# Performance work log

Measured on AMD Instinct MI355X. Metric: run time of the kernel, lower is better.

The kernel has to match this reference:

```python
import jax, jax.numpy as jnp
import numpy as np

N, K = 256, 133
INPUT_W, INPUT_H = 256, 256
SPLIT = 2.0
W = round(INPUT_W * SPLIT)  # 512
H = round(INPUT_H * SPLIT)  # 512
SIGMA = (5.66, 5.66)
BETA = 10.0
LABEL_BETA = 10.0


def setup_inputs() -> dict:
    key = jax.random.key(0)
    k1, k2, k3 = jax.random.split(key, 3)
    pred = jax.random.normal(k1, (N, K, W + H), dtype=jnp.float32)
    xy = jax.random.uniform(k2, (N, K, 2), dtype=jnp.float32) * INPUT_W
    vis = (jax.random.uniform(k3, (N, K, 1), dtype=jnp.float32) > 0.2).astype(jnp.float32)
    keypoints = jnp.concatenate([xy, vis], axis=-1)
    return {"pred": pred, "keypoints": keypoints}


def _gaussian_targets(keypoints):
    # Vectorized equivalent of the Python (n,k) loop in gaussian_smoothng.
    kp_xy = keypoints[..., :2]
    vis = keypoints[..., 2]
    mu = jnp.round(kp_xy * SPLIT)  # int64 in torch; rounded float is numerically identical
    rx = SIGMA[0] * 3.0
    ry = SIGMA[1] * 3.0
    left = mu[..., 0] - rx
    right = mu[..., 0] + rx + 1.0
    top = mu[..., 1] - ry
    bottom = mu[..., 1] + ry + 1.0
    oob = (left >= W) | (top >= H) | (right < 0) | (bottom < 0)
    visible = vis >= 0.5
    valid = visible & (~oob)
    x = jnp.arange(W, dtype=jnp.float32)
    y = jnp.arange(H, dtype=jnp.float32)
    gx = jnp.exp(-((x[None, None, :] - mu[..., 0:1]) ** 2) / (2.0 * SIGMA[0] ** 2))
    gy = jnp.exp(-((y[None, None, :] - mu[..., 1:2]) ** 2) / (2.0 * SIGMA[1] ** 2))
    target_x = jnp.where(valid[..., None], gx, 0.0)  # (N,K,W)
    target_y = jnp.where(valid[..., None], gy, 0.0)  # (N,K,H)
    # weight = visible value, zeroed if visible but out of bounds
    weight = jnp.where(visible & oob, 0.0, vis)
    return target_x, target_y, weight


def _criterion(p, t):
    # p, t: (N*K, L). KLDivLoss(reduction='none') then mean over dim=1.
    log_pt = jax.nn.log_softmax(p * BETA, axis=1)
    lab = jax.nn.softmax(t * LABEL_BETA, axis=1)  # strictly positive
    kl = lab * (jnp.log(lab) - log_pt)
    return kl.mean(axis=1)


def reference(pred, keypoints):
    n, k, _ = pred.shape
    split = pred.shape[-1] // 2
    pred_x = pred[..., :split].reshape(-1, split)
    pred_y = pred[..., split:].reshape(-1, pred.shape[-1] - split)
    gt_x, gt_y, w = _gaussian_targets(keypoints)
    w = w.reshape(-1)
    loss_x = (_criterion(pred_x, gt_x.reshape(-1, W)) * w).sum()
    loss_y = (_criterion(pred_y, gt_y.reshape(-1, H)) * w).sum()
    return (loss_x + loss_y) / k
```

## Files before the change

kernel.cpp:

```cpp
#include <hip/hip_runtime.h>
#include <math.h>

#define NKP 133
#define NROWS (256 * NKP)
#define RH_TOTAL (2 * NROWS)
#define NBLOCKS 2048
#define C2P  14.4269504088896f
#define NK2  0.02251706f

static __device__ __forceinline__ float fexp2(float x) {
    return __builtin_amdgcn_exp2f(x);
}

__global__ __launch_bounds__(256) void rtmcc_partial_kernel(
    const float* __restrict__ pred,
    const float* __restrict__ keypoints,
    float* __restrict__ partials)
{
    const int wave = threadIdx.x >> 6;
    const int lane = threadIdx.x & 63;
    const float lanef = (float)lane;
    __shared__ float lds[4];

    const float rad = 5.66f * 3.0f;
    float acc = 0.0f;

    for (int rh = blockIdx.x * 4 + wave; rh < RH_TOTAL; rh += NBLOCKS * 4) {
        const int row = rh >> 1;
        const int h   = rh & 1;

        const float kx  = keypoints[row * 3 + 0];
        const float ky  = keypoints[row * 3 + 1];
        const float vis = keypoints[row * 3 + 2];

        const float mux = rintf(kx * 2.0f);
        const float muy = rintf(ky * 2.0f);
        const bool oob = (mux - rad >= 512.0f) || (muy - rad >= 512.0f) ||
                         (mux + rad + 1.0f < 0.0f) || (muy + rad + 1.0f < 0.0f);
        const bool visible = (vis >= 0.5f);
        const float w = (visible && oob) ? 0.0f : vis;
        if (!(w > 0.0f)) continue;

        const float mu = h ? muy : mux;
        const float* pr = pred + (size_t)rh * 512;

        const float* p = pr + lane * 8;
        const float4 pa = *reinterpret_cast<const float4*>(p);
        const float4 pb = *reinterpret_cast<const float4*>(p + 4);
        const float pv[8] = {pa.x, pa.y, pa.z, pa.w, pb.x, pb.y, pb.z, pb.w};

        float S = 0.0f, P = 0.0f;
        #pragma unroll
        for (int u = 0; u < 8; ++u) {
            S += fexp2(C2P * pv[u]);
            P += pv[u];
        }

        int ws = (int)mu - 64;
        ws = ws < 0 ? 0 : (ws > 384 ? 384 : ws);
        const float pw0 = pr[ws + lane];
        const float pw1 = pr[ws + 64 + lane];
        const float d0 = ((float)ws - mu) + lanef;
        const float d1 = d0 + 64.0f;

        const float g0 = fexp2(d0 * d0 * -NK2);
        const float e0 = fexp2(g0 * C2P);
        const float g1 = fexp2(d1 * d1 * -NK2);
        const float e1 = fexp2(g1 * C2P);

        float Zw = e0 + e1;
        float Tp = e0 * g0 + e1 * g1;
        float Pd = P + (e0 - 1.0f) * pw0 + (e1 - 1.0f) * pw1;

        #pragma unroll
        for (int off = 1; off < 64; off <<= 1) {
            S  += __shfl_xor(S,  off, 64);
            Zw += __shfl_xor(Zw, off, 64);
            Tp += __shfl_xor(Tp, off, 64);
            Pd += __shfl_xor(Pd, off, 64);
        }

        const float Z = 384.0f + Zw;
        const float loss = 10.0f * (Tp - Pd) / Z + __logf(S) - __logf(Z);
        acc += w * loss;
    }

    acc *= (1.0f / (512.0f * 133.0f));
    if (lane == 0) lds[wave] = acc;
    __syncthreads();
    if (threadIdx.x == 0)
        partials[blockIdx.x] = lds[0] + lds[1] + lds[2] + lds[3];
}

__global__ __launch_bounds__(256) void rtmcc_reduce_kernel(
    const float* __restrict__ partials, float* __restrict__ out)
{
    __shared__ float lds[4];
    float s = 0.0f;
    for (int i = threadIdx.x; i < NBLOCKS; i += 256) s += partials[i];
    #pragma unroll
    for (int off = 1; off < 64; off <<= 1) s += __shfl_xor(s, off, 64);
    if ((threadIdx.x & 63) == 0) lds[threadIdx.x >> 6] = s;
    __syncthreads();
    if (threadIdx.x == 0) out[0] = lds[0] + lds[1] + lds[2] + lds[3];
}

extern "C" void kernel_launch(void* const* d_in, const int* in_sizes, int n_in,
                              void* d_out, int out_size, void* d_ws, size_t ws_size,
                              hipStream_t stream) {
    const float* pred = (const float*)d_in[0];
    const float* kpts = (const float*)d_in[1];
    float* out = (float*)d_out;
    float* partials = (float*)d_ws;

    rtmcc_partial_kernel<<<NBLOCKS, 256, 0, stream>>>(pred, kpts, partials);
    rtmcc_reduce_kernel<<<1, 256, 0, stream>>>(partials, out);
}
```

Baseline: 30.14 us.

## Software-pipeline row loads and compute gaussian window per-lane instead of gathered loads

Each wave's row loop is unrolled into a fixed trip count of eight plus a tail, with double-buffered register prefetch so the next row's keypoint and pred loads are issued before the current row is reduced. The separate 128-wide window gather from pred is removed; instead each lane computes gaussian terms for its own 8 elements only when its columns fall near mu, reusing values already in registers. This cuts the extra dependent global loads and hides memory latency, at the cost of more registers and a hardcoded row count that assumes the fixed problem size.

```diff
diff --git a/kernel.cpp b/kernel.cpp
--- a/kernel.cpp
+++ b/kernel.cpp
@@ -5,8 +5,12 @@
 #define NROWS (256 * NKP)
 #define RH_TOTAL (2 * NROWS)
 #define NBLOCKS 2048
+#define NWAVES (NBLOCKS * 4)
+#define KMAIN 8
+#define TAIL_CNT (RH_TOTAL - KMAIN * NWAVES)
 #define C2P  14.4269504088896f
 #define NK2  0.02251706f
+#define RAD  16.98f
 
 static __device__ __forceinline__ float fexp2(float x) {
     return __builtin_amdgcn_exp2f(x);
@@ -19,71 +23,79 @@
 {
     const int wave = threadIdx.x >> 6;
     const int lane = threadIdx.x & 63;
-    const float lanef = (float)lane;
+    const int wid  = blockIdx.x * 4 + wave;
+    const float c0 = (float)(lane * 8);
     __shared__ float lds[4];
 
-    const float rad = 5.66f * 3.0f;
     float acc = 0.0f;
 
-    for (int rh = blockIdx.x * 4 + wave; rh < RH_TOTAL; rh += NBLOCKS * 4) {
-        const int row = rh >> 1;
-        const int h   = rh & 1;
+#define PREP(RH, W, MU, PA, PB, GUARD)                                         \
+    {                                                                          \
+        if (GUARD) {                                                           \
+            const int row_ = (RH) >> 1;                                        \
+            const float kx_  = keypoints[row_ * 3 + 0];                        \
+            const float ky_  = keypoints[row_ * 3 + 1];                        \
+            const float vis_ = keypoints[row_ * 3 + 2];                        \
+            const float mux_ = rintf(kx_ * 2.0f);                              \
+            const float muy_ = rintf(ky_ * 2.0f);                              \
+            const bool oob_ = (mux_ - RAD >= 512.0f) || (muy_ - RAD >= 512.0f) \
+                           || (mux_ + RAD + 1.0f < 0.0f)                       \
+                           || (muy_ + RAD + 1.0f < 0.0f);                      \
+            const bool visible_ = (vis_ >= 0.5f);                              \
+            W = (visible_ && oob_) ? 0.0f : vis_;                              \
+            MU = ((RH) & 1) ? muy_ : mux_;                                     \
+            if (W > 0.0f) {                                                    \
+                const float* p_ = pred + (size_t)(RH) * 512 + lane * 8;        \
+                PA = *reinterpret_cast<const float4*>(p_);                     \
+                PB = *reinterpret_cast<const float4*>(p_ + 4);                 \
+            }                                                                  \
+        } else { W = 0.0f; }                                                   \
+    }
 
-        const float kx  = keypoints[row * 3 + 0];
-        const float ky  = keypoints[row * 3 + 1];
-        const float vis = keypoints[row * 3 + 2];
+#define COMPUTE(W, MU, PA, PB)                                                 \
+    if (W > 0.0f) {                                                            \
+        const float pv_[8] = {PA.x, PA.y, PA.z, PA.w, PB.x, PB.y, PB.z, PB.w}; \
+        float S = 0.0f, P = 0.0f;                                              \
+        _Pragma("unroll")                                                      \
+        for (int u = 0; u < 8; ++u) { S += fexp2(C2P * pv_[u]); P += pv_[u]; } \
+        float Zw = 0.0f, Tp = 0.0f, Pd = P;                                    \
+        if (c0 >= MU - 42.0f && c0 <= MU + 35.0f) {    \
+            _Pragma("unroll")                                                  \
+            for (int u = 0; u < 8; ++u) {                                      \
+                const float d_ = c0 + (float)u - MU;                           \
+                const float g_ = fexp2(d_ * d_ * -NK2);   \
+                const float e_ = fexp2(g_ * C2P);               \
+                const float em1_ = e_ - 1.0f;                                  \
+                Zw += em1_;                                                    \
+                Tp += e_ * g_;                                                 \
+                Pd += em1_ * pv_[u];                                           \
+            }                                                                  \
+        }                                                                      \
+        _Pragma("unroll")                                                      \
+        for (int off = 1; off < 64; off <<= 1) {                               \
+            S  += __shfl_xor(S,  off, 64);                                     \
+            Zw += __shfl_xor(Zw, off, 64);                                     \
+            Tp += __shfl_xor(Tp, off, 64);                                     \
+            Pd += __shfl_xor(Pd, off, 64);                                     \
+        }                                                                      \
+        const float Z = 512.0f + Zw;               \
+        acc += W * (10.0f * (Tp - Pd) / Z + __logf(S) - __logf(Z));            \
+    }
 
-        const float mux = rintf(kx * 2.0f);
-        const float muy = rintf(ky * 2.0f);
-        const bool oob = (mux - rad >= 512.0f) || (muy - rad >= 512.0f) ||
-                         (mux + rad + 1.0f < 0.0f) || (muy + rad + 1.0f < 0.0f);
-        const bool visible = (vis >= 0.5f);
-        const float w = (visible && oob) ? 0.0f : vis;
-        if (!(w > 0.0f)) continue;
+    float w0, mu0; float4 a0, b0;
+    float w1, mu1; float4 a1, b1;
 
-        const float mu = h ? muy : mux;
-        const float* pr = pred + (size_t)rh * 512;
+    PREP(wid, w0, mu0, a0, b0, true);
 
-        const float* p = pr + lane * 8;
-        const float4 pa = *reinterpret_cast<const float4*>(p);
-        const float4 pb = *reinterpret_cast<const float4*>(p + 4);
-        const float pv[8] = {pa.x, pa.y, pa.z, pa.w, pb.x, pb.y, pb.z, pb.w};
-
-        float S = 0.0f, P = 0.0f;
-        #pragma unroll
-        for (int u = 0; u < 8; ++u) {
-            S += fexp2(C2P * pv[u]);
-            P += pv[u];
-        }
-
-        int ws = (int)mu - 64;
-        ws = ws < 0 ? 0 : (ws > 384 ? 384 : ws);
-        const float pw0 = pr[ws + lane];
-        const float pw1 = pr[ws + 64 + lane];
-        const float d0 = ((float)ws - mu) + lanef;
-        const float d1 = d0 + 64.0f;
-
-        const float g0 = fexp2(d0 * d0 * -NK2);
-        const float e0 = fexp2(g0 * C2P);
-        const float g1 = fexp2(d1 * d1 * -NK2);
-        const float e1 = fexp2(g1 * C2P);
-
-        float Zw = e0 + e1;
-        float Tp = e0 * g0 + e1 * g1;
-        float Pd = P + (e0 - 1.0f) * pw0 + (e1 - 1.0f) * pw1;
-
-        #pragma unroll
-        for (int off = 1; off < 64; off <<= 1) {
-            S  += __shfl_xor(S,  off, 64);
-            Zw += __shfl_xor(Zw, off, 64);
-            Tp += __shfl_xor(Tp, off, 64);
-            Pd += __shfl_xor(Pd, off, 64);
-        }
-
-        const float Z = 384.0f + Zw;
-        const float loss = 10.0f * (Tp - Pd) / Z + __logf(S) - __logf(Z);
-        acc += w * loss;
+    #pragma unroll
+    for (int kk = 0; kk < KMAIN; kk += 2) {
+        PREP(wid + (kk + 1) * NWAVES, w1, mu1, a1, b1, true);
+        COMPUTE(w0, mu0, a0, b0);
+        PREP(wid + (kk + 2) * NWAVES, w0, mu0, a0, b0,
+             (kk + 2 < KMAIN) || (wid < TAIL_CNT));
+        COMPUTE(w1, mu1, a1, b1);
     }
+    COMPUTE(w0, mu0, a0, b0);
 
     acc *= (1.0f / (512.0f * 133.0f));
     if (lane == 0) lds[wave] = acc;
```

Result: slower. 38.30 us (+27.1%).

## Tabulate Gaussian target exponentials in LDS and prefetch next keypoint

Applied to the files above, without the earlier changes.

Each block precomputes a 256-entry shared-memory table of (e-1) and e*g for Gaussian offsets, so the per-row double exp2 becomes two table lookups. The loss algebra is regrouped to use a single shuffle-reduced term, with one fewer reduction. The next iteration's keypoints are prefetched to hide load latency. Rows that are visible but out of bounds now skip the window work, which fixes handling of the zero target. The cost is a per-block table setup plus a barrier, which adds overhead to blocks that handle few rows.

```diff
diff --git a/kernel.cpp b/kernel.cpp
--- a/kernel.cpp
+++ b/kernel.cpp
@@ -5,8 +5,11 @@
 #define NROWS (256 * NKP)
 #define RH_TOTAL (2 * NROWS)
 #define NBLOCKS 2048
+#define NWAVES (NBLOCKS * 4)
 #define C2P  14.4269504088896f
 #define NK2  0.02251706f
+#define RAD  16.98f
+#define LN2f 0.69314718055994531f
 
 static __device__ __forceinline__ float fexp2(float x) {
     return __builtin_amdgcn_exp2f(x);
@@ -19,70 +22,96 @@
 {
     const int wave = threadIdx.x >> 6;
     const int lane = threadIdx.x & 63;
-    const float lanef = (float)lane;
+    __shared__ float t_em1[256];
+    __shared__ float t_eg [256];
     __shared__ float lds[4];
 
-    const float rad = 5.66f * 3.0f;
+    {
+        const int t = threadIdx.x;
+        const float d = (float)(t - 128);
+        float em1 = 0.0f, eg = 0.0f;
+        if (fabsf(d) <= 35.0f) {
+            const float g = fexp2(-d * d * NK2);
+            const float e = fexp2(g * C2P);
+            em1 = e - 1.0f;
+            eg  = e * g;
+        }
+        t_em1[t] = em1;
+        t_eg [t] = eg;
+    }
+    __syncthreads();
+
     float acc = 0.0f;
 
-    for (int rh = blockIdx.x * 4 + wave; rh < RH_TOTAL; rh += NBLOCKS * 4) {
-        const int row = rh >> 1;
-        const int h   = rh & 1;
+    const int rh0 = blockIdx.x * 4 + wave;
+    {
+        const int r0 = rh0 >> 1;
+        float kx = keypoints[r0 * 3 + 0];
+        float ky = keypoints[r0 * 3 + 1];
+        float kv = keypoints[r0 * 3 + 2];
 
-        const float kx  = keypoints[row * 3 + 0];
-        const float ky  = keypoints[row * 3 + 1];
-        const float vis = keypoints[row * 3 + 2];
+        for (int rh = rh0; rh < RH_TOTAL; rh += NWAVES) {
+            const float kxc = kx, kyc = ky, kvc = kv;
+            const int rhn = rh + NWAVES;
+            if (rhn < RH_TOTAL) {
+                const int rn = rhn >> 1;
+                kx = keypoints[rn * 3 + 0];
+                ky = keypoints[rn * 3 + 1];
+                kv = keypoints[rn * 3 + 2];
+            }
 
-        const float mux = rintf(kx * 2.0f);
-        const float muy = rintf(ky * 2.0f);
-        const bool oob = (mux - rad >= 512.0f) || (muy - rad >= 512.0f) ||
-                         (mux + rad + 1.0f < 0.0f) || (muy + rad + 1.0f < 0.0f);
-        const bool visible = (vis >= 0.5f);
-        const float w = (visible && oob) ? 0.0f : vis;
-        if (!(w > 0.0f)) continue;
+            const float mux = rintf(kxc * 2.0f);
+            const float muy = rintf(kyc * 2.0f);
+            const bool oob = (mux - RAD >= 512.0f) || (muy - RAD >= 512.0f) ||
+                             (mux + RAD + 1.0f < 0.0f) || (muy + RAD + 1.0f < 0.0f);
+            const bool visible = (kvc >= 0.5f);
+            const float w = (visible && oob) ? 0.0f : kvc;
+            if (!(w > 0.0f)) continue;
+            const bool valid = visible && !oob;
 
-        const float mu = h ? muy : mux;
-        const float* pr = pred + (size_t)rh * 512;
+            const float mu  = (rh & 1) ? muy : mux;
+            const int   mui = (int)mu;
+            const float* pr = pred + (size_t)rh * 512;
 
-        const float* p = pr + lane * 8;
-        const float4 pa = *reinterpret_cast<const float4*>(p);
-        const float4 pb = *reinterpret_cast<const float4*>(p + 4);
-        const float pv[8] = {pa.x, pa.y, pa.z, pa.w, pb.x, pb.y, pb.z, pb.w};
+            const float* p = pr + lane * 8;
+            const float4 pa = *reinterpret_cast<const float4*>(p);
+            const float4 pb = *reinterpret_cast<const float4*>(p + 4);
+            const float pv[8] = {pa.x, pa.y, pa.z, pa.w, pb.x, pb.y, pb.z, pb.w};
 
-        float S = 0.0f, P = 0.0f;
-        #pragma unroll
-        for (int u = 0; u < 8; ++u) {
-            S += fexp2(C2P * pv[u]);
-            P += pv[u];
+            float S = 0.0f, R = 0.0f;
+            #pragma unroll
+            for (int u = 0; u < 8; ++u) {
+                S += fexp2(C2P * pv[u]);
+                R -= pv[u];
+            }
+
+            float Zw = 0.0f;
+            if (valid) {
+                int ws = mui - 64;
+                ws = ws < 0 ? 0 : (ws > 384 ? 384 : ws);
+                const float pw0 = pr[ws + lane];
+                const float pw1 = pr[ws + 64 + lane];
+                int t0 = ws + lane - mui + 128;
+                int t1 = t0 + 64;
+                t0 = t0 > 255 ? 255 : t0;
+                t1 = t1 > 255 ? 255 : t1;
+                const float em10 = t_em1[t0], eg0 = t_eg[t0];
+                const float em11 = t_em1[t1], eg1 = t_eg[t1];
+                Zw = em10 + em11;
+                R += (eg0 - em10 * pw0) + (eg1 - em11 * pw1);
+            }
+
+            #pragma unroll
+            for (int off = 1; off < 64; off <<= 1) {
+                S  += __shfl_xor(S,  off, 64);
+                Zw += __shfl_xor(Zw, off, 64);
+                R  += __shfl_xor(R,  off, 64);
+            }
+
+            const float Z = 512.0f + Zw;
+            const float loss = 10.0f * R / Z + (__log2f(S) - __log2f(Z)) * LN2f;
+            acc += w * loss;
         }
-
-        int ws = (int)mu - 64;
-        ws = ws < 0 ? 0 : (ws > 384 ? 384 : ws);
-        const float pw0 = pr[ws + lane];
-        const float pw1 = pr[ws + 64 + lane];
-        const float d0 = ((float)ws - mu) + lanef;
-        const float d1 = d0 + 64.0f;
-
-        const float g0 = fexp2(d0 * d0 * -NK2);
-        const float e0 = fexp2(g0 * C2P);
-        const float g1 = fexp2(d1 * d1 * -NK2);
-        const float e1 = fexp2(g1 * C2P);
-
-        float Zw = e0 + e1;
-        float Tp = e0 * g0 + e1 * g1;
-        float Pd = P + (e0 - 1.0f) * pw0 + (e1 - 1.0f) * pw1;
-
-        #pragma unroll
-        for (int off = 1; off < 64; off <<= 1) {
-            S  += __shfl_xor(S,  off, 64);
-            Zw += __shfl_xor(Zw, off, 64);
-            Tp += __shfl_xor(Tp, off, 64);
-            Pd += __shfl_xor(Pd, off, 64);
-        }
-
-        const float Z = 384.0f + Zw;
-        const float loss = 10.0f * (Tp - Pd) / Z + __logf(S) - __logf(Z);
-        acc += w * loss;
     }
 
     acc *= (1.0f / (512.0f * 133.0f));
```

New measurement: 29.31 us. 2.8% less time.
